# Kernel tuning notes

Measured on AMD Instinct MI355X. Metric: run time of the kernel, lower is better.

The kernel has to match this reference:

```python
import jax, jax.numpy as jnp
import numpy as np

BITA = 3  # activation bits
BITW = 1  # weight bits (binary, DoReFa sign path)


def _ste(x, q):
    """Straight-through estimator: forward = q, backward = identity wrt x."""
    return x + jax.lax.stop_gradient(q - x)


def cabs(x):
    # tl: tf.minimum(1.0, tf.abs(x))
    return jnp.minimum(1.0, jnp.abs(x))


def quantize_active(x, bitA):
    if bitA == 32:
        return x
    n = float(2 ** bitA - 1)
    # DoReFa quantize with round-STE
    return _ste(x, jnp.round(x * n) / n)


def quantize_weight(w, bitW):
    if bitW == 32:
        return w
    if bitW == 1:
        # E = stop_gradient(mean|w|); sign has identity gradient override -> STE == identity
        E = jax.lax.stop_gradient(jnp.mean(jnp.abs(w)))
        return _ste(w, jnp.sign(w / E) * E)
    # general k-bit path (not hit with defaults)
    t = jnp.tanh(w)
    t = t / jnp.max(jnp.abs(t)) * 0.5 + 0.5
    n = float(2 ** bitW - 1)
    return 2.0 * _ste(t, jnp.round(t * n) / n) - 1.0


def setup_inputs() -> dict:
    key = jax.random.key(0)
    kx, kw = jax.random.split(key)
    x = jax.random.normal(kx, (8, 512, 512, 16), dtype=jnp.float32)
    W = jax.random.normal(kw, (3, 3, 16, 32), dtype=jnp.float32) * 0.02  # trunc-normal-ish init
    b = jnp.zeros((32,), dtype=jnp.float32)
    return {"x": x, "W": W, "b": b}


def reference(x, W, b):
    # DoReFa fake-quantized activations (clip to [0,1] then 3-bit quantize, STE)
    xq = quantize_active(cabs(x), BITA)
    # DoReFa binarized weights (sign * mean|W|, STE)
    wq = quantize_weight(W, BITW)
    # full-precision conv2d, NHWC / HWIO, stride 1, SAME padding
    y = jax.lax.conv_general_dilated(
        xq, wq,
        window_strides=(1, 1),
        padding="SAME",
        dimension_numbers=("NHWC", "HWIO", "NHWC"),
    )
    y = y + b  # bias_add over channel dim; act=None
    return y
```

## Files before the change

### kernel.cpp

```cpp
#include <hip/hip_runtime.h>
#include <hip/hip_bf16.h>


typedef __bf16 bf16x8 __attribute__((ext_vector_type(8)));
typedef float f32x4 __attribute__((ext_vector_type(4)));

#define TW 32
#define TH 16
#define LW 34
#define LH 18
#define PST 48

__device__ __forceinline__ unsigned short quant3(float v) {
  float t = rintf(fminf(fabsf(v), 1.0f) * 7.0f);
  union { float f; unsigned int u; } cv; cv.f = t;
  return (unsigned short)(cv.u >> 16);
}

__global__ void prep_kernel(const float* __restrict__ W, float* __restrict__ ws) {
  __shared__ float red[256];
  int tid = threadIdx.x;
  float s = 0.f;
  for (int i = tid; i < 4608; i += 256) s += fabsf(W[i]);
  red[tid] = s;
  __syncthreads();
  for (int off = 128; off > 0; off >>= 1) {
    if (tid < off) red[tid] += red[tid + off];
    __syncthreads();
  }
  float E = red[0] * (1.0f / 4608.0f);
  if (tid == 0) ws[0] = E * (1.0f / 7.0f);
  unsigned short* bf = (unsigned short*)(ws + 4);
  for (int i = tid; i < 5 * 2 * 64 * 8; i += 256) {
    int j  = i & 7;
    int l  = (i >> 3) & 63;
    int nf = (i >> 9) & 1;
    int p  = i >> 10;
    int g  = l >> 4;
    float v = 0.f;
    if (p < 4 || g < 2) {
      int pos = (p < 4) ? (2 * p + (g >> 1)) : 8;
      int ci  = (g & 1) * 8 + j;
      int c   = nf * 16 + (l & 15);
      float w = W[(pos * 16 + ci) * 32 + c];
      v = (w > 0.f) ? 1.f : ((w < 0.f) ? -1.f : 0.f);
    }
    union { float f; unsigned int u; } cv; cv.f = v;
    bf[i] = (unsigned short)(cv.u >> 16);
  }
}

__global__ __launch_bounds__(256) void conv_kernel(
    const float* __restrict__ x, const float* __restrict__ bias,
    const float* __restrict__ ws, float* __restrict__ out) {
  __shared__ __align__(16) char lds[LH * LW * PST];
  const unsigned short* bfr = (const unsigned short*)(ws + 4);

  int bid = blockIdx.x;
  int tile_x = bid & 15;
  int tile_y = (bid >> 4) & 31;
  int n      = bid >> 9;
  int gx0 = tile_x * TW, gy0 = tile_y * TH;
  int tid  = threadIdx.x;
  int lane = tid & 63;
  int wv   = tid >> 6;
  int g    = lane >> 4;
  int m    = lane & 15;

  bf16x8 bfrag[5][2];
#pragma unroll
  for (int p = 0; p < 5; ++p)
#pragma unroll
    for (int nf = 0; nf < 2; ++nf)
      bfrag[p][nf] = *(const bf16x8*)(bfr + ((p * 2 + nf) * 64 + lane) * 8);
  float scale = ws[0];
  float4 bias0 = ((const float4*)bias)[g];
  float4 bias1 = ((const float4*)bias)[g + 4];

  const float* xn = x + (size_t)n * (512 * 512 * 16);
  for (int i = tid; i < LH * LW * 4; i += 256) {
    int cig = i & 3;
    int pix = i >> 2;
    int py = pix / LW;
    int px = pix - py * LW;
    int gy = gy0 - 1 + py, gx = gx0 - 1 + px;
    float4 v = make_float4(0.f, 0.f, 0.f, 0.f);
    if (gy >= 0 && gy < 512 && gx >= 0 && gx < 512)
      v = *(const float4*)(xn + ((gy << 9) + gx) * 16 + cig * 4);
    ushort4 q;
    q.x = quant3(v.x); q.y = quant3(v.y); q.z = quant3(v.z); q.w = quant3(v.w);
    *(ushort4*)(&lds[pix * PST + cig * 8]) = q;
  }

  int laneoff[5];
#pragma unroll
  for (int p = 0; p < 5; ++p) {
    int pos = (p < 4) ? (2 * p + (g >> 1)) : 8;
    int kh = pos / 3, kw = pos - kh * 3;
    laneoff[p] = (kh * LW + kw) * PST + (g & 1) * 16 + m * PST;
  }

  __syncthreads();

#pragma unroll
  for (int r = 0; r < 4; ++r) {
    int ty = wv * 4 + r;
#pragma unroll
    for (int xt = 0; xt < 2; ++xt) {
      int tx = xt * 16;
      int base = (ty * LW + tx) * PST;
      f32x4 acc0 = {0.f, 0.f, 0.f, 0.f};
      f32x4 acc1 = {0.f, 0.f, 0.f, 0.f};
#pragma unroll
      for (int p = 0; p < 5; ++p) {
        bf16x8 b = *(const bf16x8*)(&lds[base + laneoff[p]]);
        acc0 = __builtin_amdgcn_mfma_f32_16x16x32_bf16(bfrag[p][0], b, acc0, 0, 0, 0);
        acc1 = __builtin_amdgcn_mfma_f32_16x16x32_bf16(bfrag[p][1], b, acc1, 0, 0, 0);
      }
      float4 o0, o1;
      o0.x = acc0[0] * scale + bias0.x;  o0.y = acc0[1] * scale + bias0.y;
      o0.z = acc0[2] * scale + bias0.z;  o0.w = acc0[3] * scale + bias0.w;
      o1.x = acc1[0] * scale + bias1.x;  o1.y = acc1[1] * scale + bias1.y;
      o1.z = acc1[2] * scale + bias1.z;  o1.w = acc1[3] * scale + bias1.w;
      float* op = out + (((size_t)((n << 9) + (gy0 + ty)) << 9) + (gx0 + tx + m)) * 32 + (g << 2);
      *(float4*)op = o0;
      *(float4*)(op + 16) = o1;
    }
  }
}

extern "C" void kernel_launch(void* const* d_in, const int* in_sizes, int n_in,
                              void* d_out, int out_size, void* d_ws, size_t ws_size,
                              hipStream_t stream) {
  const float* x = (const float*)d_in[0];
  const float* W = (const float*)d_in[1];
  const float* b = (const float*)d_in[2];
  float* out = (float*)d_out;
  float* ws  = (float*)d_ws;

  prep_kernel<<<1, 256, 0, stream>>>(W, ws);
  conv_kernel<<<4096, 256, 0, stream>>>(x, b, ws, out);
}
```

Baseline: 392.7 us.

## Make conv blocks persistent over 8 row tiles with double-buffered LDS prefetch

Each block now processes 8 vertically stacked tiles instead of one. The next tile's global loads are held in registers while MFMA work runs on the current LDS buffer, so load latency can overlap compute, and the grid drops from 4096 to 512 blocks. The weight fragment column order is permuted so each lane writes 8 contiguous output channels as two adjacent float4s. The cost is more LDS and registers per block and fewer blocks in flight on the GPU, which may reduce latency hiding.

```diff
diff --git a/kernel.cpp b/kernel.cpp
--- a/kernel.cpp
+++ b/kernel.cpp
@@ -10,6 +10,10 @@
 #define LW 34
 #define LH 18
 #define PST 48
+#define NPIX (LH * LW)
+#define NLD  (NPIX * 4)
+#define NIT  10
+#define NT   8
 
 __device__ __forceinline__ unsigned short quant3(float v) {
   float t = rintf(fminf(fabsf(v), 1.0f) * 7.0f);
@@ -37,11 +41,12 @@
     int nf = (i >> 9) & 1;
     int p  = i >> 10;
     int g  = l >> 4;
+    int r  = l & 15;
     float v = 0.f;
     if (p < 4 || g < 2) {
       int pos = (p < 4) ? (2 * p + (g >> 1)) : 8;
       int ci  = (g & 1) * 8 + j;
-      int c   = nf * 16 + (l & 15);
+      int c   = ((r >> 2) << 3) + (r & 3) + nf * 4;
       float w = W[(pos * 16 + ci) * 32 + c];
       v = (w > 0.f) ? 1.f : ((w < 0.f) ? -1.f : 0.f);
     }
@@ -53,14 +58,14 @@
 __global__ __launch_bounds__(256) void conv_kernel(
     const float* __restrict__ x, const float* __restrict__ bias,
     const float* __restrict__ ws, float* __restrict__ out) {
-  __shared__ __align__(16) char lds[LH * LW * PST];
+  __shared__ __align__(16) char lds[2][NPIX * PST];
   const unsigned short* bfr = (const unsigned short*)(ws + 4);
 
   int bid = blockIdx.x;
-  int tile_x = bid & 15;
-  int tile_y = (bid >> 4) & 31;
-  int n      = bid >> 9;
-  int gx0 = tile_x * TW, gy0 = tile_y * TH;
+  int tyg = bid & 3;
+  int txt = (bid >> 2) & 15;
+  int n   = bid >> 6;
+  int gx0 = txt * TW;
   int tid  = threadIdx.x;
   int lane = tid & 63;
   int wv   = tid >> 6;
@@ -74,23 +79,10 @@
     for (int nf = 0; nf < 2; ++nf)
       bfrag[p][nf] = *(const bf16x8*)(bfr + ((p * 2 + nf) * 64 + lane) * 8);
   float scale = ws[0];
-  float4 bias0 = ((const float4*)bias)[g];
-  float4 bias1 = ((const float4*)bias)[g + 4];
+  float4 bias0 = ((const float4*)bias)[2 * g];
+  float4 bias1 = ((const float4*)bias)[2 * g + 1];
 
   const float* xn = x + (size_t)n * (512 * 512 * 16);
-  for (int i = tid; i < LH * LW * 4; i += 256) {
-    int cig = i & 3;
-    int pix = i >> 2;
-    int py = pix / LW;
-    int px = pix - py * LW;
-    int gy = gy0 - 1 + py, gx = gx0 - 1 + px;
-    float4 v = make_float4(0.f, 0.f, 0.f, 0.f);
-    if (gy >= 0 && gy < 512 && gx >= 0 && gx < 512)
-      v = *(const float4*)(xn + ((gy << 9) + gx) * 16 + cig * 4);
-    ushort4 q;
-    q.x = quant3(v.x); q.y = quant3(v.y); q.z = quant3(v.z); q.w = quant3(v.w);
-    *(ushort4*)(&lds[pix * PST + cig * 8]) = q;
-  }
 
   int laneoff[5];
 #pragma unroll
@@ -100,32 +92,76 @@
     laneoff[p] = (kh * LW + kw) * PST + (g & 1) * 16 + m * PST;
   }
 
-  __syncthreads();
+  float4 sreg[NIT];
 
+  auto issue_loads = [&](int t) {
+    int gy0 = (tyg * NT + t) * TH;
 #pragma unroll
-  for (int r = 0; r < 4; ++r) {
-    int ty = wv * 4 + r;
+    for (int it = 0; it < NIT; ++it) {
+      int i = tid + it * 256;
+      float4 v = make_float4(0.f, 0.f, 0.f, 0.f);
+      if (i < NLD) {
+        int cig = i & 3;
+        int pix = i >> 2;
+        int py = pix / LW;
+        int px = pix - py * LW;
+        int gy = gy0 - 1 + py, gx = gx0 - 1 + px;
+        if (gy >= 0 && gy < 512 && gx >= 0 && gx < 512)
+          v = *(const float4*)(xn + ((gy << 9) + gx) * 16 + cig * 4);
+      }
+      sreg[it] = v;
+    }
+  };
+
+  auto write_tile = [&](int buf) {
 #pragma unroll
-    for (int xt = 0; xt < 2; ++xt) {
-      int tx = xt * 16;
-      int base = (ty * LW + tx) * PST;
-      f32x4 acc0 = {0.f, 0.f, 0.f, 0.f};
-      f32x4 acc1 = {0.f, 0.f, 0.f, 0.f};
+    for (int it = 0; it < NIT; ++it) {
+      int i = tid + it * 256;
+      if (i < NLD) {
+        int cig = i & 3;
+        int pix = i >> 2;
+        ushort4 q;
+        q.x = quant3(sreg[it].x); q.y = quant3(sreg[it].y);
+        q.z = quant3(sreg[it].z); q.w = quant3(sreg[it].w);
+        *(ushort4*)(&lds[buf][pix * PST + cig * 8]) = q;
+      }
+    }
+  };
+
+  issue_loads(0);
+  write_tile(0);
+
+  for (int t = 0; t < NT; ++t) {
+    __syncthreads();
+    if (t + 1 < NT) issue_loads(t + 1);
+    int gy0 = (tyg * NT + t) * TH;
+    const char* buf = lds[t & 1];
 #pragma unroll
-      for (int p = 0; p < 5; ++p) {
-        bf16x8 b = *(const bf16x8*)(&lds[base + laneoff[p]]);
-        acc0 = __builtin_amdgcn_mfma_f32_16x16x32_bf16(bfrag[p][0], b, acc0, 0, 0, 0);
-        acc1 = __builtin_amdgcn_mfma_f32_16x16x32_bf16(bfrag[p][1], b, acc1, 0, 0, 0);
+    for (int r = 0; r < 4; ++r) {
+      int ty = wv * 4 + r;
+#pragma unroll
+      for (int xt = 0; xt < 2; ++xt) {
+        int tx = xt * 16;
+        int base = (ty * LW + tx) * PST;
+        f32x4 acc0 = {0.f, 0.f, 0.f, 0.f};
+        f32x4 acc1 = {0.f, 0.f, 0.f, 0.f};
+#pragma unroll
+        for (int p = 0; p < 5; ++p) {
+          bf16x8 b = *(const bf16x8*)(&buf[base + laneoff[p]]);
+          acc0 = __builtin_amdgcn_mfma_f32_16x16x32_bf16(bfrag[p][0], b, acc0, 0, 0, 0);
+          acc1 = __builtin_amdgcn_mfma_f32_16x16x32_bf16(bfrag[p][1], b, acc1, 0, 0, 0);
+        }
+        float4 o0, o1;
+        o0.x = acc0[0] * scale + bias0.x;  o0.y = acc0[1] * scale + bias0.y;
+        o0.z = acc0[2] * scale + bias0.z;  o0.w = acc0[3] * scale + bias0.w;
+        o1.x = acc1[0] * scale + bias1.x;  o1.y = acc1[1] * scale + bias1.y;
+        o1.z = acc1[2] * scale + bias1.z;  o1.w = acc1[3] * scale + bias1.w;
+        float* op = out + (((size_t)((n << 9) + (gy0 + ty)) << 9) + (gx0 + tx + m)) * 32 + (g << 3);
+        *(float4*)op = o0;
+        *(float4*)(op + 4) = o1;
       }
-      float4 o0, o1;
-      o0.x = acc0[0] * scale + bias0.x;  o0.y = acc0[1] * scale + bias0.y;
-      o0.z = acc0[2] * scale + bias0.z;  o0.w = acc0[3] * scale + bias0.w;
-      o1.x = acc1[0] * scale + bias1.x;  o1.y = acc1[1] * scale + bias1.y;
-      o1.z = acc1[2] * scale + bias1.z;  o1.w = acc1[3] * scale + bias1.w;
-      float* op = out + (((size_t)((n << 9) + (gy0 + ty)) << 9) + (gx0 + tx + m)) * 32 + (g << 2);
-      *(float4*)op = o0;
-      *(float4*)(op + 16) = o1;
     }
+    if (t + 1 < NT) write_tile((t + 1) & 1);
   }
 }
 
@@ -139,5 +175,5 @@
   float* ws  = (float*)d_ws;
 
   prep_kernel<<<1, 256, 0, stream>>>(W, ws);
-  conv_kernel<<<4096, 256, 0, stream>>>(x, b, ws, out);
+  conv_kernel<<<512, 256, 0, stream>>>(x, b, ws, out);
 }
```

After: 416.4 us. 1.06x slower.
